# Kernel tuning notes

Measured on AMD Instinct MI355X. Metric: run time of the kernel, lower is better.

Reference implementation:

```python
import jax, jax.numpy as jnp
import numpy as np

D = 1024
M = 4096


def _linear_params(key, fan_in, fan_out):
    kw, kb = jax.random.split(key)
    bound = 1.0 / np.sqrt(fan_in)
    W = jax.random.uniform(kw, (fan_out, fan_in), jnp.float32, -bound, bound)
    b = jax.random.uniform(kb, (fan_out,), jnp.float32, -bound, bound)
    return W, b


def setup_inputs() -> dict:
    key = jax.random.key(0)
    ks = jax.random.split(key, 6)
    x = jax.random.normal(ks[0], (4, 2048, D), jnp.float32)
    Wq, bq = _linear_params(ks[1], D, D)
    Wk, bk = _linear_params(ks[2], D, D)
    Wv, bv = _linear_params(ks[3], D, D)
    Wo, bo = _linear_params(ks[4], D, D)
    Wf, bf = _linear_params(ks[5], D, M)
    return {"x": x, "Wq": Wq, "bq": bq, "Wk": Wk, "bk": bk,
            "Wv": Wv, "bv": bv, "Wo": Wo, "bo": bo, "Wf": Wf, "bf": bf}


def reference(x, Wq, bq, Wk, bk, Wv, bv, Wo, bo, Wf, bf):
    # projections (torch Linear: x @ W.T + b)
    Q = x @ Wq.T + bq  # [B,S,D]
    K = x @ Wk.T + bk
    V = x @ Wv.T + bv
    d_k = Q.shape[-1]
    scores = jnp.einsum('bqd,bkd->bqk', Q, K) / jnp.sqrt(jnp.float32(d_k))
    S = scores.shape[-1]
    causal = jnp.tril(jnp.ones((S, S), dtype=bool))  # [S,S]
    scores = jnp.where(causal, scores, -jnp.inf)
    probs = jax.nn.softmax(scores, axis=-1)
    attn = jnp.einsum('bqk,bkd->bqd', probs, V)
    out = attn @ Wo.T + bo
    # FFN: Linear(d->m) + GELU (torch default: exact erf GELU)
    ff = jax.nn.gelu(out @ Wf.T + bf, approximate=False)
    return ff
```

## Files before the change

kernel.cpp:

```cpp
#include <hip/hip_runtime.h>
#include <hip/hip_bf16.h>
#include <math.h>

using bf16 = __hip_bfloat16;
typedef __attribute__((ext_vector_type(8))) short bf16x8;
typedef __attribute__((ext_vector_type(4))) short bf16x4;
typedef __attribute__((ext_vector_type(4))) float f32x4;

#define GLOBAL_AS __attribute__((address_space(1)))
#define LDS_AS __attribute__((address_space(3)))

__device__ __forceinline__ float b2f(bf16 v) { return __bfloat162float(v); }
__device__ __forceinline__ bf16 f2b(float v) { return __float2bfloat16(v); }

__device__ __forceinline__ float gelu_f(float x) {
  float u = x * (0.7978845608f + 0.0356774081f * x * x);
  float t = 1.0f - 2.0f / (1.0f + __expf(2.0f * u));
  return 0.5f * x * (1.0f + t);
}

__global__ __launch_bounds__(256) void k_conv(const float* __restrict__ src,
                                              bf16* __restrict__ dst, int n4) {
  int i = blockIdx.x * 256 + threadIdx.x;
  if (i >= n4) return;
  float4 v = ((const float4*)src)[i];
  bf16 t[4] = {f2b(v.x), f2b(v.y), f2b(v.z), f2b(v.w)};
  *(bf16x4*)(dst + 4 * (size_t)i) = *(bf16x4*)t;
}

__device__ __forceinline__ void stage_async(const bf16* __restrict__ g,
                                            int ldg, bf16* __restrict__ s) {
  int lane = threadIdx.x & 63;
  int wave = threadIdx.x >> 6;
  bf16* lds = s + wave * 1024;
  const bf16* g0 = g + (size_t)(wave * 32 + (lane >> 2)) * ldg + ((lane & 3) << 3);
  const bf16* g1 = g0 + (size_t)16 * ldg;
  __builtin_amdgcn_global_load_lds((GLOBAL_AS const unsigned*)g0,
                                   (LDS_AS unsigned*)lds, 16, 0, 0);
  __builtin_amdgcn_global_load_lds((GLOBAL_AS const unsigned*)g1,
                                   (LDS_AS unsigned*)(lds + 512), 16, 0, 0);
}

struct Acc { f32x4 a[4][4]; };

__device__ __forceinline__ void gemm_core(const bf16* __restrict__ A,
                                          const bf16* __restrict__ B,
                                          int K, int lda, int ldb, Acc& acc,
                                          bf16* sA, bf16* sB) {
  int lane = threadIdx.x & 63;
  int wave = threadIdx.x >> 6;
  int wm = wave & 1, wn = wave >> 1;
  int r = lane & 15;
  int ko = (lane >> 4) << 3;

  for (int k0 = 0; k0 < K; k0 += 64) {
    stage_async(A + k0,      lda, sA);
    stage_async(A + k0 + 32, lda, sA + 4096);
    stage_async(B + k0,      ldb, sB);
    stage_async(B + k0 + 32, ldb, sB + 4096);
    __syncthreads();
#pragma unroll
    for (int kk = 0; kk < 2; ++kk) {
      bf16x8 af[4], bfr[4];
#pragma unroll
      for (int t = 0; t < 4; ++t) {
        af[t]  = *(const bf16x8*)(sA + kk * 4096 + (wm * 64 + t * 16 + r) * 32 + ko);
        bfr[t] = *(const bf16x8*)(sB + kk * 4096 + (wn * 64 + t * 16 + r) * 32 + ko);
      }
#pragma unroll
      for (int tm = 0; tm < 4; ++tm)
#pragma unroll
        for (int tn = 0; tn < 4; ++tn)
          acc.a[tm][tn] = __builtin_amdgcn_mfma_f32_16x16x32_bf16(
              af[tm], bfr[tn], acc.a[tm][tn], 0, 0, 0);
    }
    __syncthreads();
  }
}

template <typename TO, bool BIAS, bool GELU>
__device__ __forceinline__ void epilogue(const Acc& acc, TO* __restrict__ C,
                                         int ldc, const float* __restrict__ bias,
                                         float scale) {
  int lane = threadIdx.x & 63;
  int wave = threadIdx.x >> 6;
  int wm = wave & 1, wn = wave >> 1;
  int rbase = wm * 64 + ((lane >> 4) << 2);
  int cbase = wn * 64 + (lane & 15);
#pragma unroll
  for (int tm = 0; tm < 4; ++tm) {
#pragma unroll
    for (int tn = 0; tn < 4; ++tn) {
      int nn = cbase + tn * 16;
      float bv = BIAS ? bias[nn] : 0.0f;
#pragma unroll
      for (int rr = 0; rr < 4; ++rr) {
        int mm = rbase + tm * 16 + rr;
        float c = acc.a[tm][tn][rr] * scale + bv;
        if (GELU) c = gelu_f(c);
        if constexpr (__hip_internal::is_same<TO, bf16>::value)
          C[(size_t)mm * ldc + nn] = f2b(c);
        else
          C[(size_t)mm * ldc + nn] = c;
      }
    }
  }
}

__global__ __launch_bounds__(256) void k_qkv(
    const bf16* __restrict__ X, const bf16* __restrict__ Wq,
    const bf16* __restrict__ Wk, const bf16* __restrict__ Wv,
    const float* __restrict__ bq, const float* __restrict__ bk,
    const float* __restrict__ bv,
    bf16* __restrict__ Q, bf16* __restrict__ Ko, bf16* __restrict__ Vt) {
  __shared__ alignas(16) char arena[32768];
  bf16* sA = (bf16*)arena;
  bf16* sB = (bf16*)(arena + 16384);
  const int K = 1024, N = 1024;
  int z = blockIdx.z;
  const bf16* W     = (z == 0) ? Wq : (z == 1) ? Wk : Wv;
  const float* bias = (z == 0) ? bq : (z == 1) ? bk : bv;
  const bf16* A = X + (size_t)blockIdx.x * 128 * K;
  const bf16* B = W + (size_t)blockIdx.y * 128 * K;
  Acc acc = {};
  gemm_core(A, B, K, K, K, acc, sA, sB);

  if (z < 2) {
    bf16* C = (z == 0 ? Q : Ko) +
              (size_t)blockIdx.x * 128 * N + blockIdx.y * 128;
    epilogue<bf16, true, false>(acc, C, N, bias + blockIdx.y * 128, 1.0f);
  } else {
    bf16* sT = (bf16*)arena;
    int tid = threadIdx.x;
    int lane = tid & 63;
    int wave = tid >> 6;
    int wm = wave & 1, wn = wave >> 1;
    int b  = blockIdx.x >> 4;
    int s0 = (blockIdx.x & 15) * 128;
#pragma unroll
    for (int p = 0; p < 2; ++p) {
      __syncthreads();
      if (wn == p) {
        int rloc_s = wm * 64 + ((lane >> 4) << 2);
#pragma unroll
        for (int tn = 0; tn < 4; ++tn) {
          int nl = (lane & 15) + tn * 16;
          float bvv = bias[blockIdx.y * 128 + p * 64 + nl];
#pragma unroll
          for (int tm = 0; tm < 4; ++tm)
#pragma unroll
            for (int rr = 0; rr < 4; ++rr)
              sT[nl * 136 + rloc_s + tm * 16 + rr] =
                  f2b(acc.a[tm][tn][rr] + bvv);
        }
      }
      __syncthreads();
      int c = tid & 15, r0 = tid >> 4;
#pragma unroll
      for (int j = 0; j < 4; ++j) {
        int rl = r0 + j * 16;
        int n = blockIdx.y * 128 + p * 64 + rl;
        *(bf16x8*)(Vt + ((size_t)b * 1024 + n) * 2048 + s0 + c * 8) =
            *(const bf16x8*)(sT + rl * 136 + c * 8);
      }
    }
  }
}

__global__ __launch_bounds__(256) void k_scores(const bf16* __restrict__ Q,
                                                const bf16* __restrict__ Kk,
                                                bf16* __restrict__ P) {
  int bx = 15 - blockIdx.x;
  if ((int)blockIdx.y > bx) return;
  __shared__ alignas(16) char arena[32768];
  bf16* sA = (bf16*)arena;
  bf16* sB = (bf16*)(arena + 16384);
  const int K = 1024, S = 2048;
  int z = blockIdx.z;
  const bf16* A = Q  + (size_t)z * S * K + (size_t)bx * 128 * K;
  const bf16* B = Kk + (size_t)z * S * K + (size_t)blockIdx.y * 128 * K;
  Acc acc = {};
  gemm_core(A, B, K, K, K, acc, sA, sB);
  bf16* C = P + (size_t)z * S * S + (size_t)bx * 128 * S + blockIdx.y * 128;
  epilogue<bf16, false, false>(acc, C, S, nullptr, 0.03125f);
}

__global__ __launch_bounds__(256) void k_softmax(bf16* __restrict__ P) {
  const int S = 2048;
  int q = blockIdx.x, z = blockIdx.y;
  bf16* row = P + ((size_t)z * S + q) * S;
  __shared__ float red[4];
  int tid = threadIdx.x;

  float mx = -1e30f;
  for (int k = tid; k <= q; k += 256) mx = fmaxf(mx, b2f(row[k]));
#pragma unroll
  for (int o = 32; o > 0; o >>= 1) mx = fmaxf(mx, __shfl_xor(mx, o));
  if ((tid & 63) == 0) red[tid >> 6] = mx;
  __syncthreads();
  mx = fmaxf(fmaxf(red[0], red[1]), fmaxf(red[2], red[3]));
  __syncthreads();

  float sum = 0.0f;
  for (int k = tid; k <= q; k += 256) sum += __expf(b2f(row[k]) - mx);
#pragma unroll
  for (int o = 32; o > 0; o >>= 1) sum += __shfl_xor(sum, o);
  if ((tid & 63) == 0) red[tid >> 6] = sum;
  __syncthreads();
  sum = red[0] + red[1] + red[2] + red[3];
  float inv = 1.0f / sum;

  int kcap = ((q >> 7) + 1) << 7;
  for (int k = tid; k < kcap; k += 256) {
    float p = (k <= q) ? __expf(b2f(row[k]) - mx) * inv : 0.0f;
    row[k] = f2b(p);
  }
}

__global__ __launch_bounds__(256) void k_attn(const bf16* __restrict__ P,
                                              const bf16* __restrict__ Vt,
                                              bf16* __restrict__ O) {
  __shared__ alignas(16) char arena[32768];
  bf16* sA = (bf16*)arena;
  bf16* sB = (bf16*)(arena + 16384);
  const int S = 2048, D = 1024;
  int bx = 15 - (int)blockIdx.x;
  int z = blockIdx.z;
  int Keff = (bx + 1) * 128;
  const bf16* A = P  + (size_t)z * S * S + (size_t)bx * 128 * S;
  const bf16* B = Vt + (size_t)z * D * S + (size_t)blockIdx.y * 128 * S;
  Acc acc = {};
  gemm_core(A, B, Keff, S, S, acc, sA, sB);
  bf16* C = O + (size_t)z * S * D + (size_t)bx * 128 * D + blockIdx.y * 128;
  epilogue<bf16, false, false>(acc, C, D, nullptr, 1.0f);
}

__global__ __launch_bounds__(256) void k_out(const bf16* __restrict__ A0,
                                             const bf16* __restrict__ W,
                                             const float* __restrict__ bias,
                                             bf16* __restrict__ C0) {
  __shared__ alignas(16) char arena[32768];
  bf16* sA = (bf16*)arena;
  bf16* sB = (bf16*)(arena + 16384);
  const int K = 1024, N = 1024;
  const bf16* A = A0 + (size_t)blockIdx.x * 128 * K;
  const bf16* B = W + (size_t)blockIdx.y * 128 * K;
  Acc acc = {};
  gemm_core(A, B, K, K, K, acc, sA, sB);
  bf16* C = C0 + (size_t)blockIdx.x * 128 * N + blockIdx.y * 128;
  epilogue<bf16, true, false>(acc, C, N, bias + blockIdx.y * 128, 1.0f);
}

__global__ __launch_bounds__(256) void k_ffn(const bf16* __restrict__ A0,
                                             const bf16* __restrict__ W,
                                             const float* __restrict__ bias,
                                             float* __restrict__ C0) {
  __shared__ alignas(16) char arena[32768];
  bf16* sA = (bf16*)arena;
  bf16* sB = (bf16*)(arena + 16384);
  const int K = 1024, N = 4096;
  const bf16* A = A0 + (size_t)blockIdx.x * 128 * K;
  const bf16* B = W + (size_t)blockIdx.y * 128 * K;
  Acc acc = {};
  gemm_core(A, B, K, K, K, acc, sA, sB);
  float* C = C0 + (size_t)blockIdx.x * 128 * N + blockIdx.y * 128;
  epilogue<float, true, true>(acc, C, N, bias + blockIdx.y * 128, 1.0f);
}

extern "C" void kernel_launch(void* const* d_in, const int* in_sizes, int n_in,
                              void* d_out, int out_size, void* d_ws,
                              size_t ws_size, hipStream_t stream) {
  const float* x   = (const float*)d_in[0];
  const float* Wq  = (const float*)d_in[1];
  const float* bq  = (const float*)d_in[2];
  const float* Wk  = (const float*)d_in[3];
  const float* bk  = (const float*)d_in[4];
  const float* Wv  = (const float*)d_in[5];
  const float* bv  = (const float*)d_in[6];
  const float* Wo  = (const float*)d_in[7];
  const float* bo  = (const float*)d_in[8];
  const float* Wf  = (const float*)d_in[9];
  const float* bfb = (const float*)d_in[10];

  char* ws = (char*)d_ws;
  const size_t MB = 1 << 20;
  bf16* xb   = (bf16*)(ws);
  bf16* Wqb  = (bf16*)(ws + 16 * MB);
  bf16* Wkb  = (bf16*)(ws + 18 * MB);
  bf16* Wvb  = (bf16*)(ws + 20 * MB);
  bf16* P    = (bf16*)(ws);
  bf16* Q    = (bf16*)(ws + 32 * MB);
  bf16* Kb   = (bf16*)(ws + 48 * MB);
  bf16* Wob  = (bf16*)(ws + 48 * MB);
  bf16* Wfb  = (bf16*)(ws + 50 * MB);
  bf16* Vt   = (bf16*)(ws + 64 * MB);
  bf16* attn = Q;
  bf16* out  = Vt;
  float* y   = (float*)d_out;

  k_conv<<<8192, 256, 0, stream>>>(x,  xb,  8192 * 1024 / 4);
  k_conv<<<1024, 256, 0, stream>>>(Wq, Wqb, 1024 * 1024 / 4);
  k_conv<<<1024, 256, 0, stream>>>(Wk, Wkb, 1024 * 1024 / 4);
  k_conv<<<1024, 256, 0, stream>>>(Wv, Wvb, 1024 * 1024 / 4);
  k_qkv<<<dim3(64, 8, 3), 256, 0, stream>>>(xb, Wqb, Wkb, Wvb, bq, bk, bv,
                                            Q, Kb, Vt);
  k_scores<<<dim3(16, 16, 4), 256, 0, stream>>>(Q, Kb, P);
  k_conv<<<1024, 256, 0, stream>>>(Wo, Wob, 1024 * 1024 / 4);
  k_conv<<<4096, 256, 0, stream>>>(Wf, Wfb, 4096 * 1024 / 4);
  k_softmax<<<dim3(2048, 4), 256, 0, stream>>>(P);
  k_attn<<<dim3(16, 8, 4), 256, 0, stream>>>(P, Vt, attn);
  k_out<<<dim3(64, 8), 256, 0, stream>>>(attn, Wob, bo, out);
  k_ffn<<<dim3(64, 32), 256, 0, stream>>>(out, Wfb, bfb, y);
}
```

Before: 508.3 us.

## Halve GEMM K-step to cut LDS, vectorize softmax, merge conversion launches

The shared GEMM core now stages 32-wide K slices instead of 64, which halves the LDS arena per block so more blocks can be resident per CU. The cost is twice as many barriers per K-loop. Softmax rows are now read and written in 8-element bf16 vectors instead of scalars, reducing memory transactions. The six separate fp32-to-bf16 conversion launches are merged into two launches to cut launch overhead.

```diff
diff --git a/kernel.cpp b/kernel.cpp
--- a/kernel.cpp
+++ b/kernel.cpp
@@ -12,6 +12,11 @@
 
 __device__ __forceinline__ float b2f(bf16 v) { return __bfloat162float(v); }
 __device__ __forceinline__ bf16 f2b(float v) { return __float2bfloat16(v); }
+__device__ __forceinline__ float bs2f(short s) {
+  union { unsigned u; float f; } x;
+  x.u = ((unsigned)(unsigned short)s) << 16;
+  return x.f;
+}
 
 __device__ __forceinline__ float gelu_f(float x) {
   float u = x * (0.7978845608f + 0.0356774081f * x * x);
@@ -19,10 +24,37 @@
   return 0.5f * x * (1.0f + t);
 }
 
-__global__ __launch_bounds__(256) void k_conv(const float* __restrict__ src,
-                                              bf16* __restrict__ dst, int n4) {
-  int i = blockIdx.x * 256 + threadIdx.x;
-  if (i >= n4) return;
+__global__ __launch_bounds__(256) void k_conv4(
+    const float* __restrict__ x, const float* __restrict__ Wq,
+    const float* __restrict__ Wk, const float* __restrict__ Wv,
+    bf16* __restrict__ xb, bf16* __restrict__ Wqb,
+    bf16* __restrict__ Wkb, bf16* __restrict__ Wvb) {
+  int bid = blockIdx.x;
+  const float* src;
+  bf16* dst;
+  int local;
+  if (bid < 8192) { src = x; dst = xb; local = bid; }
+  else {
+    int b2 = bid - 8192;
+    int w = b2 >> 10;
+    local = b2 & 1023;
+    src = (w == 0) ? Wq : (w == 1) ? Wk : Wv;
+    dst = (w == 0) ? Wqb : (w == 1) ? Wkb : Wvb;
+  }
+  int i = local * 256 + threadIdx.x;
+  float4 v = ((const float4*)src)[i];
+  bf16 t[4] = {f2b(v.x), f2b(v.y), f2b(v.z), f2b(v.w)};
+  *(bf16x4*)(dst + 4 * (size_t)i) = *(bf16x4*)t;
+}
+
+__global__ __launch_bounds__(256) void k_conv2(
+    const float* __restrict__ Wo, const float* __restrict__ Wf,
+    bf16* __restrict__ Wob, bf16* __restrict__ Wfb) {
+  int bid = blockIdx.x;
+  const float* src = (bid < 1024) ? Wo : Wf;
+  bf16* dst = (bid < 1024) ? Wob : Wfb;
+  int local = (bid < 1024) ? bid : bid - 1024;
+  int i = local * 256 + threadIdx.x;
   float4 v = ((const float4*)src)[i];
   bf16 t[4] = {f2b(v.x), f2b(v.y), f2b(v.z), f2b(v.w)};
   *(bf16x4*)(dst + 4 * (size_t)i) = *(bf16x4*)t;
@@ -53,27 +85,22 @@
   int r = lane & 15;
   int ko = (lane >> 4) << 3;
 
-  for (int k0 = 0; k0 < K; k0 += 64) {
-    stage_async(A + k0,      lda, sA);
-    stage_async(A + k0 + 32, lda, sA + 4096);
-    stage_async(B + k0,      ldb, sB);
-    stage_async(B + k0 + 32, ldb, sB + 4096);
+  for (int k0 = 0; k0 < K; k0 += 32) {
+    stage_async(A + k0, lda, sA);
+    stage_async(B + k0, ldb, sB);
     __syncthreads();
-#pragma unroll
-    for (int kk = 0; kk < 2; ++kk) {
-      bf16x8 af[4], bfr[4];
-#pragma unroll
-      for (int t = 0; t < 4; ++t) {
-        af[t]  = *(const bf16x8*)(sA + kk * 4096 + (wm * 64 + t * 16 + r) * 32 + ko);
-        bfr[t] = *(const bf16x8*)(sB + kk * 4096 + (wn * 64 + t * 16 + r) * 32 + ko);
-      }
-#pragma unroll
-      for (int tm = 0; tm < 4; ++tm)
-#pragma unroll
-        for (int tn = 0; tn < 4; ++tn)
-          acc.a[tm][tn] = __builtin_amdgcn_mfma_f32_16x16x32_bf16(
-              af[tm], bfr[tn], acc.a[tm][tn], 0, 0, 0);
+    bf16x8 af[4], bfr[4];
+#pragma unroll
+    for (int t = 0; t < 4; ++t) {
+      af[t]  = *(const bf16x8*)(sA + (wm * 64 + t * 16 + r) * 32 + ko);
+      bfr[t] = *(const bf16x8*)(sB + (wn * 64 + t * 16 + r) * 32 + ko);
     }
+#pragma unroll
+    for (int tm = 0; tm < 4; ++tm)
+#pragma unroll
+      for (int tn = 0; tn < 4; ++tn)
+        acc.a[tm][tn] = __builtin_amdgcn_mfma_f32_16x16x32_bf16(
+            af[tm], bfr[tn], acc.a[tm][tn], 0, 0, 0);
     __syncthreads();
   }
 }
@@ -113,9 +140,9 @@
     const float* __restrict__ bq, const float* __restrict__ bk,
     const float* __restrict__ bv,
     bf16* __restrict__ Q, bf16* __restrict__ Ko, bf16* __restrict__ Vt) {
-  __shared__ alignas(16) char arena[32768];
-  bf16* sA = (bf16*)arena;
-  bf16* sB = (bf16*)(arena + 16384);
+  __shared__ alignas(16) char arena[17408];
+  bf16* sA = (bf16*)arena;
+  bf16* sB = (bf16*)(arena + 8192);
   const int K = 1024, N = 1024;
   int z = blockIdx.z;
   const bf16* W     = (z == 0) ? Wq : (z == 1) ? Wk : Wv;
@@ -172,9 +199,9 @@
                                                 bf16* __restrict__ P) {
   int bx = 15 - blockIdx.x;
   if ((int)blockIdx.y > bx) return;
-  __shared__ alignas(16) char arena[32768];
-  bf16* sA = (bf16*)arena;
-  bf16* sB = (bf16*)(arena + 16384);
+  __shared__ alignas(16) char arena[16384];
+  bf16* sA = (bf16*)arena;
+  bf16* sB = (bf16*)(arena + 8192);
   const int K = 1024, S = 2048;
   int z = blockIdx.z;
   const bf16* A = Q  + (size_t)z * S * K + (size_t)bx * 128 * K;
@@ -191,9 +218,17 @@
   bf16* row = P + ((size_t)z * S + q) * S;
   __shared__ float red[4];
   int tid = threadIdx.x;
+  int kcap = ((q >> 7) + 1) << 7;
+  int nch = kcap >> 3;
 
   float mx = -1e30f;
-  for (int k = tid; k <= q; k += 256) mx = fmaxf(mx, b2f(row[k]));
+  for (int c = tid; c < nch; c += 256) {
+    int k = c << 3;
+    bf16x8 v = *(const bf16x8*)(row + k);
+#pragma unroll
+    for (int j = 0; j < 8; ++j)
+      if (k + j <= q) mx = fmaxf(mx, bs2f(v[j]));
+  }
 #pragma unroll
   for (int o = 32; o > 0; o >>= 1) mx = fmaxf(mx, __shfl_xor(mx, o));
   if ((tid & 63) == 0) red[tid >> 6] = mx;
@@ -202,7 +237,13 @@
   __syncthreads();
 
   float sum = 0.0f;
-  for (int k = tid; k <= q; k += 256) sum += __expf(b2f(row[k]) - mx);
+  for (int c = tid; c < nch; c += 256) {
+    int k = c << 3;
+    bf16x8 v = *(const bf16x8*)(row + k);
+#pragma unroll
+    for (int j = 0; j < 8; ++j)
+      if (k + j <= q) sum += __expf(bs2f(v[j]) - mx);
+  }
 #pragma unroll
   for (int o = 32; o > 0; o >>= 1) sum += __shfl_xor(sum, o);
   if ((tid & 63) == 0) red[tid >> 6] = sum;
@@ -210,19 +251,25 @@
   sum = red[0] + red[1] + red[2] + red[3];
   float inv = 1.0f / sum;
 
-  int kcap = ((q >> 7) + 1) << 7;
-  for (int k = tid; k < kcap; k += 256) {
-    float p = (k <= q) ? __expf(b2f(row[k]) - mx) * inv : 0.0f;
-    row[k] = f2b(p);
+  for (int c = tid; c < nch; c += 256) {
+    int k = c << 3;
+    bf16x8 v = *(const bf16x8*)(row + k);
+    bf16 t[8];
+#pragma unroll
+    for (int j = 0; j < 8; ++j) {
+      float p = (k + j <= q) ? __expf(bs2f(v[j]) - mx) * inv : 0.0f;
+      t[j] = f2b(p);
+    }
+    *(bf16x8*)(row + k) = *(bf16x8*)t;
   }
 }
 
 __global__ __launch_bounds__(256) void k_attn(const bf16* __restrict__ P,
                                               const bf16* __restrict__ Vt,
                                               bf16* __restrict__ O) {
-  __shared__ alignas(16) char arena[32768];
-  bf16* sA = (bf16*)arena;
-  bf16* sB = (bf16*)(arena + 16384);
+  __shared__ alignas(16) char arena[16384];
+  bf16* sA = (bf16*)arena;
+  bf16* sB = (bf16*)(arena + 8192);
   const int S = 2048, D = 1024;
   int bx = 15 - (int)blockIdx.x;
   int z = blockIdx.z;
@@ -239,9 +286,9 @@
                                              const bf16* __restrict__ W,
                                              const float* __restrict__ bias,
                                              bf16* __restrict__ C0) {
-  __shared__ alignas(16) char arena[32768];
-  bf16* sA = (bf16*)arena;
-  bf16* sB = (bf16*)(arena + 16384);
+  __shared__ alignas(16) char arena[16384];
+  bf16* sA = (bf16*)arena;
+  bf16* sB = (bf16*)(arena + 8192);
   const int K = 1024, N = 1024;
   const bf16* A = A0 + (size_t)blockIdx.x * 128 * K;
   const bf16* B = W + (size_t)blockIdx.y * 128 * K;
@@ -255,9 +302,9 @@
                                              const bf16* __restrict__ W,
                                              const float* __restrict__ bias,
                                              float* __restrict__ C0) {
-  __shared__ alignas(16) char arena[32768];
-  bf16* sA = (bf16*)arena;
-  bf16* sB = (bf16*)(arena + 16384);
+  __shared__ alignas(16) char arena[16384];
+  bf16* sA = (bf16*)arena;
+  bf16* sB = (bf16*)(arena + 8192);
   const int K = 1024, N = 4096;
   const bf16* A = A0 + (size_t)blockIdx.x * 128 * K;
   const bf16* B = W + (size_t)blockIdx.y * 128 * K;
@@ -298,15 +345,11 @@
   bf16* out  = Vt;
   float* y   = (float*)d_out;
 
-  k_conv<<<8192, 256, 0, stream>>>(x,  xb,  8192 * 1024 / 4);
-  k_conv<<<1024, 256, 0, stream>>>(Wq, Wqb, 1024 * 1024 / 4);
-  k_conv<<<1024, 256, 0, stream>>>(Wk, Wkb, 1024 * 1024 / 4);
-  k_conv<<<1024, 256, 0, stream>>>(Wv, Wvb, 1024 * 1024 / 4);
+  k_conv4<<<11264, 256, 0, stream>>>(x, Wq, Wk, Wv, xb, Wqb, Wkb, Wvb);
   k_qkv<<<dim3(64, 8, 3), 256, 0, stream>>>(xb, Wqb, Wkb, Wvb, bq, bk, bv,
                                             Q, Kb, Vt);
   k_scores<<<dim3(16, 16, 4), 256, 0, stream>>>(Q, Kb, P);
-  k_conv<<<1024, 256, 0, stream>>>(Wo, Wob, 1024 * 1024 / 4);
-  k_conv<<<4096, 256, 0, stream>>>(Wf, Wfb, 4096 * 1024 / 4);
+  k_conv2<<<5120, 256, 0, stream>>>(Wo, Wf, Wob, Wfb);
   k_softmax<<<dim3(2048, 4), 256, 0, stream>>>(P);
   k_attn<<<dim3(16, 8, 4), 256, 0, stream>>>(P, Vt, attn);
   k_out<<<dim3(64, 8), 256, 0, stream>>>(attn, Wob, bo, out);
```

Result: faster. 495.4 us (-2.5%).
